# Optimization experiments

Measured on AMD Instinct MI355X. Metric: run time of the kernel, lower is better.

## Reference

```python
import jax, jax.numpy as jnp
import numpy as np

V, T, E, H, L = 32000, 1024, 1024, 16, 6
D = E // H
FF = 4 * E
B = 2


def _ln(x, s, b, eps=1e-5):
    m = x.mean(-1, keepdims=True)
    v = x.var(-1, keepdims=True)
    return (x - m) * jax.lax.rsqrt(v + eps) * s + b


def setup_inputs() -> dict:
    key = jax.random.key(0)
    ks = jax.random.split(key, 16)
    std = 0.02
    inp = {
        "idx": jax.random.randint(ks[0], (B, T), 0, V),
        "tok_w": jax.random.normal(ks[1], (V, E)) * std,
        "pos_emb": jax.random.normal(ks[2], (1, T, E)) * std,
        # stacked per-layer params [L, ...]
        "ln1_s": jnp.ones((L, E)), "ln1_b": jnp.zeros((L, E)),
        "wq": jax.random.normal(ks[3], (L, E, E)) * std,
        "wk": jax.random.normal(ks[4], (L, E, E)) * std,
        "wv": jax.random.normal(ks[5], (L, E, E)) * std,
        "wo": jax.random.normal(ks[6], (L, E, E)) * std,
        "bo": jnp.zeros((L, E)),
        "ln2_s": jnp.ones((L, E)), "ln2_b": jnp.zeros((L, E)),
        "w1": jax.random.normal(ks[7], (L, E, FF)) * std,
        "b1": jnp.zeros((L, FF)),
        "w2": jax.random.normal(ks[8], (L, FF, E)) * std,
        "b2": jnp.zeros((L, E)),
        "lnf_s": jnp.ones((E,)), "lnf_b": jnp.zeros((E,)),
        "head_w": jax.random.normal(ks[9], (E, V)) * std,
        "head_b": jnp.zeros((V,)),
    }
    return inp


def _gpt(idx, tok_w, pos_emb, ln1_s, ln1_b, wq, wk, wv, wo, bo,
         ln2_s, ln2_b, w1, b1, w2, b2, lnf_s, lnf_b, head_w, head_b):
    x = tok_w[idx] + pos_emb[0, :T]                      # [B,T,E]
    mask = jnp.tril(jnp.ones((T, T), dtype=bool))        # causal mask
    scale = 1.0 / np.sqrt(D)

    def step(x, p):
        l1s, l1b, q_w, k_w, v_w, o_w, o_b, l2s, l2b, f1, fb1, f2, fb2 = p
        h = _ln(x, l1s, l1b)
        q = (h @ q_w).reshape(B, T, H, D)
        k = (h @ k_w).reshape(B, T, H, D)
        v = (h @ v_w).reshape(B, T, H, D)
        att = jnp.einsum('bthd,bshd->bhts', q, k) * scale  # [B,H,T,T]
        att = jnp.where(mask, att, -jnp.inf)
        att = jax.nn.softmax(att, axis=-1)
        o = jnp.einsum('bhts,bshd->bthd', att, v).reshape(B, T, E)
        x = x + o @ o_w + o_b
        h2 = _ln(x, l2s, l2b)
        x = x + jax.nn.relu(h2 @ f1 + fb1) @ f2 + fb2
        return x, None

    params = (ln1_s, ln1_b, wq, wk, wv, wo, bo, ln2_s, ln2_b, w1, b1, w2, b2)
    x, _ = jax.lax.scan(step, x, params)
    x = _ln(x, lnf_s, lnf_b)
    return x @ head_w + head_b                           # logits [B,T,V]


def reference(idx, tok_w, pos_emb, ln1_s, ln1_b, wq, wk, wv, wo, bo,
              ln2_s, ln2_b, w1, b1, w2, b2, lnf_s, lnf_b, head_w, head_b):
    return _gpt(idx, tok_w, pos_emb, ln1_s, ln1_b, wq, wk, wv, wo, bo,
                ln2_s, ln2_b, w1, b1, w2, b2, lnf_s, lnf_b, head_w, head_b)
```

## Files before the change

### kernel.cpp

```cpp
#include <hip/hip_runtime.h>


#define T_SEQ 1024
#define E_DIM 1024
#define H_NUM 16
#define D_HEAD 64
#define L_NUM 6
#define FF_DIM 4096
#define B_NUM 2
#define M_ROWS 2048

using bf16x8 = __attribute__((ext_vector_type(8))) __bf16;
using f32x4  = __attribute__((ext_vector_type(4))) float;

__device__ __forceinline__ unsigned short f2bf(float f) {
  unsigned int u = __float_as_uint(f);
  u += 0x7fffu + ((u >> 16) & 1u);
  return (unsigned short)(u >> 16);
}

__device__ __forceinline__ void gload_lds16(const void* g, void* l) {
  __builtin_amdgcn_global_load_lds(
      (const __attribute__((address_space(1))) unsigned int*)g,
      (__attribute__((address_space(3))) unsigned int*)l, 16, 0, 0);
}

__global__ __launch_bounds__(256) void embed_k(const int* __restrict__ idx,
                                               const float* __restrict__ tok_w,
                                               const float* __restrict__ pos,
                                               float* __restrict__ x) {
  const int i = blockIdx.x;
  const int t = i & (T_SEQ - 1);
  const int tok = idx[i];
  const float4 a = ((const float4*)(tok_w + (size_t)tok * E_DIM))[threadIdx.x];
  const float4 p = ((const float4*)(pos + (size_t)t * E_DIM))[threadIdx.x];
  float4 o;
  o.x = a.x + p.x; o.y = a.y + p.y; o.z = a.z + p.z; o.w = a.w + p.w;
  ((float4*)(x + (size_t)i * E_DIM))[threadIdx.x] = o;
}

__global__ __launch_bounds__(256) void ln_k(const float* __restrict__ x,
                                            const float* __restrict__ s,
                                            const float* __restrict__ b,
                                            unsigned short* __restrict__ out) {
  const int row = blockIdx.x, tid = threadIdx.x;
  const float4 v = ((const float4*)(x + (size_t)row * E_DIM))[tid];
  float sum = v.x + v.y + v.z + v.w;
  float sq  = v.x * v.x + v.y * v.y + v.z * v.z + v.w * v.w;
  #pragma unroll
  for (int off = 32; off; off >>= 1) {
    sum += __shfl_down(sum, off);
    sq  += __shfl_down(sq, off);
  }
  __shared__ float sm[10];
  const int wave = tid >> 6, lane = tid & 63;
  if (lane == 0) { sm[wave] = sum; sm[4 + wave] = sq; }
  __syncthreads();
  if (tid == 0) {
    const float ts = sm[0] + sm[1] + sm[2] + sm[3];
    const float tq = sm[4] + sm[5] + sm[6] + sm[7];
    const float mean = ts * (1.0f / E_DIM);
    const float var = tq * (1.0f / E_DIM) - mean * mean;
    sm[8] = mean;
    sm[9] = 1.0f / sqrtf(var + 1e-5f);
  }
  __syncthreads();
  const float mean = sm[8], inv = sm[9];
  const float4 sv = ((const float4*)s)[tid];
  const float4 bv = ((const float4*)b)[tid];
  ushort4 o;
  o.x = f2bf((v.x - mean) * inv * sv.x + bv.x);
  o.y = f2bf((v.y - mean) * inv * sv.y + bv.y);
  o.z = f2bf((v.z - mean) * inv * sv.z + bv.z);
  o.w = f2bf((v.w - mean) * inv * sv.w + bv.w);
  *(ushort4*)(out + (size_t)row * E_DIM + (tid << 2)) = o;
}

__global__ __launch_bounds__(256) void transpose_k(const float* __restrict__ W,
                                                   unsigned short* __restrict__ WT,
                                                   int K, int ldw) {
  __shared__ float tile[32][33];
  const int n0 = blockIdx.x << 5, k0 = blockIdx.y << 5;
  const int tx = threadIdx.x & 31, ty = threadIdx.x >> 5;
  #pragma unroll
  for (int i = ty; i < 32; i += 8)
    tile[i][tx] = W[(size_t)(k0 + i) * ldw + n0 + tx];
  __syncthreads();
  #pragma unroll
  for (int i = ty; i < 32; i += 8)
    WT[(size_t)(n0 + i) * K + k0 + tx] = f2bf(tile[tx][i]);
}

template<int BM, bool RELU, bool BIAS, bool RES, bool OBF16>
__global__ __launch_bounds__(256) void gemm_k(const unsigned short* __restrict__ A,
                                              const unsigned short* __restrict__ WT,
                                              const float* __restrict__ bias,
                                              const float* __restrict__ res,
                                              void* __restrict__ Cout,
                                              int ldc, int K) {
  constexpr int BN = 128;
  constexpr int BK = 64;
  constexpr int MF = BM / 32;
  constexpr int AJ = (BM * BK * 2 / 1024) / 4;
  constexpr int BJ = (BN * BK * 2 / 1024) / 4;
  __shared__ __align__(16) unsigned short As[2][BM][BK];
  __shared__ __align__(16) unsigned short Bs[2][BN][BK];
  const int tid = threadIdx.x;
  const int row0 = blockIdx.x * BM, col0 = blockIdx.y * BN;
  const int wave = tid >> 6, lane = tid & 63;
  const int wm = (wave >> 1) * (BM / 2), wn = (wave & 1) * 64;
  const int lr = lane & 15, lg = lane >> 4;
  const int ric = lane >> 3;
  const int sslot = lane & 7;

  auto stage = [&](int buf, int k0) {
    #pragma unroll
    for (int j = 0; j < AJ; ++j) {
      const int c = wave + 4 * j;
      const int row = c * 8 + ric;
      const int sp = sslot ^ (row & 7);
      gload_lds16(A + (size_t)(row0 + row) * K + k0 + sp * 8,
                  (char*)&As[buf][0][0] + c * 1024);
    }
    #pragma unroll
    for (int j = 0; j < BJ; ++j) {
      const int c = wave + 4 * j;
      const int row = c * 8 + ric;
      const int sp = sslot ^ (row & 7);
      gload_lds16(WT + (size_t)(col0 + row) * K + k0 + sp * 8,
                  (char*)&Bs[buf][0][0] + c * 1024);
    }
  };

  f32x4 acc[MF][4] = {};
  const int nt = K / BK;
  stage(0, 0);
  __syncthreads();
  for (int t = 0; t < nt; ++t) {
    const int cur = t & 1;
    if (t + 1 < nt) stage(cur ^ 1, (t + 1) * BK);
    #pragma unroll
    for (int ks = 0; ks < 2; ++ks) {
      bf16x8 af[MF], bfr[4];
      #pragma unroll
      for (int m = 0; m < MF; ++m) {
        const int r = wm + m * 16 + lr;
        const int s = (ks * 4 + lg) ^ (r & 7);
        af[m] = *(const bf16x8*)((const char*)&As[cur][0][0] + r * 128 + s * 16);
      }
      #pragma unroll
      for (int n = 0; n < 4; ++n) {
        const int r = wn + n * 16 + lr;
        const int s = (ks * 4 + lg) ^ (r & 7);
        bfr[n] = *(const bf16x8*)((const char*)&Bs[cur][0][0] + r * 128 + s * 16);
      }
      #pragma unroll
      for (int m = 0; m < MF; ++m)
        #pragma unroll
        for (int n = 0; n < 4; ++n)
          acc[m][n] = __builtin_amdgcn_mfma_f32_16x16x32_bf16(af[m], bfr[n], acc[m][n], 0, 0, 0);
    }
    __syncthreads();
  }
  float* Cf = (float*)Cout;
  unsigned short* Cb = (unsigned short*)Cout;
  #pragma unroll
  for (int m = 0; m < MF; ++m) {
    #pragma unroll
    for (int n = 0; n < 4; ++n) {
      const int col = col0 + wn + (n << 4) + lr;
      const float bv = BIAS ? bias[col] : 0.0f;
      #pragma unroll
      for (int r = 0; r < 4; ++r) {
        const int row = row0 + wm + (m << 4) + (lg << 2) + r;
        float val = acc[m][n][r] + bv;
        if (RELU) val = fmaxf(val, 0.0f);
        if (RES)  val += res[(size_t)row * ldc + col];
        if (OBF16) Cb[(size_t)row * ldc + col] = f2bf(val);
        else       Cf[(size_t)row * ldc + col] = val;
      }
    }
  }
}

#define QBLK 64
#define KBLK 64
__global__ __launch_bounds__(256) void fattn_k(const unsigned short* __restrict__ qkv,
                                               unsigned short* __restrict__ ob) {
  const int qt = blockIdx.x, h = blockIdx.y, b = blockIdx.z;
  const int tid = threadIdx.x;
  const int wave = tid >> 6, lane = tid & 63;
  const int lr = lane & 15, lg = lane >> 4;
  const int q0 = qt * QBLK;

  __shared__ __align__(16) unsigned short Qs[QBLK][72];
  __shared__ __align__(16) unsigned short Ks[KBLK][72];
  __shared__ __align__(16) unsigned short Vt[D_HEAD][72];
  __shared__ __align__(16) unsigned short Ps[QBLK][72];

  const size_t base = (size_t)b * T_SEQ * 3072 + (size_t)h * 64;
  const int srow = tid >> 3, scol = (tid & 7) << 3;

  #pragma unroll
  for (int it = 0; it < 2; ++it) {
    const int row = srow + it * 32;
    *(uint4*)&Qs[row][scol] =
        *(const uint4*)(qkv + base + (size_t)(q0 + row) * 3072 + scol);
  }
  __syncthreads();
  bf16x8 qf[2];
  #pragma unroll
  for (int ks = 0; ks < 2; ++ks)
    qf[ks] = *(const bf16x8*)&Qs[wave * 16 + lr][ks * 32 + lg * 8];

  f32x4 acc_o[4] = {};
  float mrow[4], lrow[4];
  #pragma unroll
  for (int r = 0; r < 4; ++r) { mrow[r] = -3.0e38f; lrow[r] = 0.f; }

  const int ntile = qt + 1;
  for (int kt = 0; kt < ntile; ++kt) {
    const int s0 = kt * KBLK;
    __syncthreads();
    #pragma unroll
    for (int it = 0; it < 2; ++it) {
      const int row = srow + it * 32;
      *(uint4*)&Ks[row][scol] =
          *(const uint4*)(qkv + base + 1024 + (size_t)(s0 + row) * 3072 + scol);
      uint4 v4 = *(const uint4*)(qkv + base + 2048 + (size_t)(s0 + row) * 3072 + scol);
      const unsigned short* vs = (const unsigned short*)&v4;
      #pragma unroll
      for (int j = 0; j < 8; ++j) Vt[scol + j][row] = vs[j];
    }
    __syncthreads();

    f32x4 sacc[4] = {};
    #pragma unroll
    for (int ks = 0; ks < 2; ++ks) {
      #pragma unroll
      for (int nf = 0; nf < 4; ++nf) {
        bf16x8 kf = *(const bf16x8*)&Ks[nf * 16 + lr][ks * 32 + lg * 8];
        sacc[nf] = __builtin_amdgcn_mfma_f32_16x16x32_bf16(qf[ks], kf, sacc[nf], 0, 0, 0);
      }
    }
    float sv[4][4];
    #pragma unroll
    for (int nf = 0; nf < 4; ++nf)
      #pragma unroll
      for (int r = 0; r < 4; ++r) sv[nf][r] = sacc[nf][r] * 0.125f;
    if (kt == ntile - 1) {
      #pragma unroll
      for (int nf = 0; nf < 4; ++nf) {
        const int s = s0 + nf * 16 + lr;
        #pragma unroll
        for (int r = 0; r < 4; ++r) {
          const int q = q0 + wave * 16 + lg * 4 + r;
          if (s > q) sv[nf][r] = -3.0e38f;
        }
      }
    }
    float p[4][4];
    #pragma unroll
    for (int r = 0; r < 4; ++r) {
      float mx = fmaxf(fmaxf(sv[0][r], sv[1][r]), fmaxf(sv[2][r], sv[3][r]));
      #pragma unroll
      for (int off = 1; off < 16; off <<= 1) mx = fmaxf(mx, __shfl_xor(mx, off));
      const float mnew = fmaxf(mrow[r], mx);
      const float alpha = __expf(mrow[r] - mnew);
      mrow[r] = mnew;
      float sum = 0.f;
      #pragma unroll
      for (int nf = 0; nf < 4; ++nf) {
        p[nf][r] = __expf(sv[nf][r] - mnew);
        sum += p[nf][r];
      }
      #pragma unroll
      for (int off = 1; off < 16; off <<= 1) sum += __shfl_xor(sum, off);
      lrow[r] = lrow[r] * alpha + sum;
      #pragma unroll
      for (int df = 0; df < 4; ++df) acc_o[df][r] *= alpha;
    }
    #pragma unroll
    for (int nf = 0; nf < 4; ++nf)
      #pragma unroll
      for (int r = 0; r < 4; ++r)
        Ps[wave * 16 + lg * 4 + r][nf * 16 + lr] = f2bf(p[nf][r]);
    __syncthreads();
    #pragma unroll
    for (int ks = 0; ks < 2; ++ks) {
      bf16x8 pa = *(const bf16x8*)&Ps[wave * 16 + lr][ks * 32 + lg * 8];
      #pragma unroll
      for (int df = 0; df < 4; ++df) {
        bf16x8 vf = *(const bf16x8*)&Vt[df * 16 + lr][ks * 32 + lg * 8];
        acc_o[df] = __builtin_amdgcn_mfma_f32_16x16x32_bf16(pa, vf, acc_o[df], 0, 0, 0);
      }
    }
  }
  #pragma unroll
  for (int r = 0; r < 4; ++r) {
    const float inv = 1.0f / lrow[r];
    const int row = q0 + wave * 16 + lg * 4 + r;
    #pragma unroll
    for (int df = 0; df < 4; ++df)
      ob[((size_t)b * T_SEQ + row) * E_DIM + h * 64 + df * 16 + lr] =
          f2bf(acc_o[df][r] * inv);
  }
}

extern "C" void kernel_launch(void* const* d_in, const int* in_sizes, int n_in,
                              void* d_out, int out_size, void* d_ws, size_t ws_size,
                              hipStream_t stream) {
  (void)in_sizes; (void)n_in; (void)out_size; (void)ws_size;
  const int*   idx    = (const int*)d_in[0];
  const float* tok_w  = (const float*)d_in[1];
  const float* pos    = (const float*)d_in[2];
  const float* ln1_s  = (const float*)d_in[3];
  const float* ln1_b  = (const float*)d_in[4];
  const float* wq     = (const float*)d_in[5];
  const float* wk     = (const float*)d_in[6];
  const float* wv     = (const float*)d_in[7];
  const float* wo     = (const float*)d_in[8];
  const float* bo     = (const float*)d_in[9];
  const float* ln2_s  = (const float*)d_in[10];
  const float* ln2_b  = (const float*)d_in[11];
  const float* w1     = (const float*)d_in[12];
  const float* b1     = (const float*)d_in[13];
  const float* w2     = (const float*)d_in[14];
  const float* b2     = (const float*)d_in[15];
  const float* lnf_s  = (const float*)d_in[16];
  const float* lnf_b  = (const float*)d_in[17];
  const float* head_w = (const float*)d_in[18];
  const float* head_b = (const float*)d_in[19];
  float* out = (float*)d_out;

  char* p = (char*)d_ws;
  float* x            = (float*)p;          p += (size_t)M_ROWS * E_DIM * 4;
  unsigned short* qkvb= (unsigned short*)p; p += (size_t)M_ROWS * 3072 * 4;
  unsigned short* h   = (unsigned short*)p; p += (size_t)M_ROWS * E_DIM * 2;
  unsigned short* obuf= (unsigned short*)p; p += (size_t)M_ROWS * E_DIM * 2;
  unsigned short* ff  = (unsigned short*)p; p += (size_t)M_ROWS * FF_DIM * 2;
  unsigned short* wt  = (unsigned short*)p; p += (size_t)32000 * E_DIM * 2;

  embed_k<<<M_ROWS, 256, 0, stream>>>(idx, tok_w, pos, x);

  for (int l = 0; l < L_NUM; ++l) {
    const size_t lEE = (size_t)l * E_DIM * E_DIM;
    const size_t lEF = (size_t)l * E_DIM * FF_DIM;
    ln_k<<<M_ROWS, 256, 0, stream>>>(x, ln1_s + l * E_DIM, ln1_b + l * E_DIM, h);
    transpose_k<<<dim3(32, 32), 256, 0, stream>>>(wq + lEE, wt,               E_DIM, E_DIM);
    transpose_k<<<dim3(32, 32), 256, 0, stream>>>(wk + lEE, wt + 1048576,     E_DIM, E_DIM);
    transpose_k<<<dim3(32, 32), 256, 0, stream>>>(wv + lEE, wt + 2097152,     E_DIM, E_DIM);
    gemm_k<128,false,false,false,true><<<dim3(16, 24), 256, 0, stream>>>(
        h, wt, nullptr, nullptr, qkvb, 3072, E_DIM);
    fattn_k<<<dim3(T_SEQ / QBLK, H_NUM, B_NUM), 256, 0, stream>>>(qkvb, obuf);
    transpose_k<<<dim3(32, 32), 256, 0, stream>>>(wo + lEE, wt, E_DIM, E_DIM);
    gemm_k<64,false,true,true,false><<<dim3(32, 8), 256, 0, stream>>>(
        obuf, wt, bo + l * E_DIM, x, x, E_DIM, E_DIM);
    ln_k<<<M_ROWS, 256, 0, stream>>>(x, ln2_s + l * E_DIM, ln2_b + l * E_DIM, h);
    transpose_k<<<dim3(128, 32), 256, 0, stream>>>(w1 + lEF, wt, E_DIM, FF_DIM);
    gemm_k<128,true,true,false,true><<<dim3(16, 32), 256, 0, stream>>>(
        h, wt, b1 + l * FF_DIM, nullptr, ff, FF_DIM, E_DIM);
    transpose_k<<<dim3(32, 128), 256, 0, stream>>>(w2 + lEF, wt, FF_DIM, E_DIM);
    gemm_k<64,false,true,true,false><<<dim3(32, 8), 256, 0, stream>>>(
        ff, wt, b2 + l * E_DIM, x, x, E_DIM, FF_DIM);
  }

  ln_k<<<M_ROWS, 256, 0, stream>>>(x, lnf_s, lnf_b, h);
  transpose_k<<<dim3(1000, 32), 256, 0, stream>>>(head_w, wt, E_DIM, 32000);
  gemm_k<128,false,true,false,false><<<dim3(16, 250), 256, 0, stream>>>(
      h, wt, head_b, nullptr, out, 32000, E_DIM);
}
```

Before: 1.525 ms.

## Batch weight transposes up front and add 256x256 8-wave GEMM for LM head

All per-layer weight transposes are now done by batched launches (grid z over layers) before the layer loop, writing into dedicated per-layer transposed buffers instead of one reused scratch buffer. This cuts the number of small launches interleaved with compute. The LM head GEMM moves to a new 512-thread kernel with 256x256 tiles, quarter-split LDS double buffering, XCD-aware block remapping and MFMA priority hints, aimed at better operand reuse on the largest GEMM. The cost is a larger workspace and a more complex barrier and waitcnt schedule that must hold across the split stages.

```diff
diff --git a/kernel.cpp b/kernel.cpp
--- a/kernel.cpp
+++ b/kernel.cpp
@@ -76,15 +76,19 @@
   *(ushort4*)(out + (size_t)row * E_DIM + (tid << 2)) = o;
 }
 
-__global__ __launch_bounds__(256) void transpose_k(const float* __restrict__ W,
+__global__ __launch_bounds__(256) void transpose_b(const float* __restrict__ W,
                                                    unsigned short* __restrict__ WT,
-                                                   int K, int ldw) {
+                                                   int K, int N,
+                                                   size_t Wstride, size_t WTstride) {
   __shared__ float tile[32][33];
+  const int z = blockIdx.z;
+  W  += (size_t)z * Wstride;
+  WT += (size_t)z * WTstride;
   const int n0 = blockIdx.x << 5, k0 = blockIdx.y << 5;
   const int tx = threadIdx.x & 31, ty = threadIdx.x >> 5;
   #pragma unroll
   for (int i = ty; i < 32; i += 8)
-    tile[i][tx] = W[(size_t)(k0 + i) * ldw + n0 + tx];
+    tile[i][tx] = W[(size_t)(k0 + i) * N + n0 + tx];
   __syncthreads();
   #pragma unroll
   for (int i = ty; i < 32; i += 8)
@@ -110,8 +114,7 @@
   const int wave = tid >> 6, lane = tid & 63;
   const int wm = (wave >> 1) * (BM / 2), wn = (wave & 1) * 64;
   const int lr = lane & 15, lg = lane >> 4;
-  const int ric = lane >> 3;
-  const int sslot = lane & 7;
+  const int ric = lane >> 3, sslot = lane & 7;
 
   auto stage = [&](int buf, int k0) {
     #pragma unroll
@@ -181,6 +184,135 @@
       }
     }
   }
+}
+
+#define LOAD_AF(HALF)                                                         \
+  _Pragma("unroll")                                                           \
+  for (int mf = 0; mf < 4; ++mf) {                                            \
+    const int rr = wm * 64 + mf * 16 + lr;                                    \
+    _Pragma("unroll")                                                         \
+    for (int ks = 0; ks < 2; ++ks)                                            \
+      af[mf][ks] = *(const bf16x8*)&As[buf][HALF][rr]                         \
+          [(((ks << 2) + lgp) ^ (rr & 7)) << 3];                              \
+  }
+#define LOAD_BF(HALF)                                                         \
+  _Pragma("unroll")                                                           \
+  for (int nf = 0; nf < 2; ++nf) {                                            \
+    const int rr = wn * 32 + nf * 16 + lr;                                    \
+    _Pragma("unroll")                                                         \
+    for (int ks = 0; ks < 2; ++ks)                                            \
+      bfq[nf][ks] = *(const bf16x8*)&Bs[buf][HALF][rr]                        \
+          [(((ks << 2) + lgp) ^ (rr & 7)) << 3];                              \
+  }
+#define MFMA_Q(MH, NH)                                                        \
+  __builtin_amdgcn_s_setprio(1);                                              \
+  _Pragma("unroll")                                                           \
+  for (int mf = 0; mf < 4; ++mf)                                              \
+    _Pragma("unroll")                                                         \
+    for (int nf = 0; nf < 2; ++nf) {                                          \
+      acc[MH][NH][mf][nf] = __builtin_amdgcn_mfma_f32_16x16x32_bf16(          \
+          af[mf][0], bfq[nf][0], acc[MH][NH][mf][nf], 0, 0, 0);               \
+      acc[MH][NH][mf][nf] = __builtin_amdgcn_mfma_f32_16x16x32_bf16(          \
+          af[mf][1], bfq[nf][1], acc[MH][NH][mf][nf], 0, 0, 0);               \
+    }                                                                         \
+  __builtin_amdgcn_s_setprio(0);
+
+__global__ __launch_bounds__(512) void gemm8_k(
+    const unsigned short* __restrict__ A, const unsigned short* __restrict__ WT,
+    const float* __restrict__ bias, float* __restrict__ C,
+    int ldc, int K, int mgrid) {
+  constexpr int BK = 64;
+  __shared__ __align__(16) unsigned short As[2][2][128][64];
+  __shared__ __align__(16) unsigned short Bs[2][2][128][64];
+  const int tid = threadIdx.x;
+  const int wave = tid >> 6, lane = tid & 63;
+  const int wm = wave >> 2, wn = wave & 3;
+  const int lr = lane & 15, lgp = lane >> 4;
+  const int nwg = gridDim.x;
+  const int q = nwg >> 3, r = nwg & 7;
+  const int xcd = blockIdx.x & 7;
+  const int lgid = (xcd < r ? xcd * (q + 1) : r * (q + 1) + (xcd - r) * q)
+                   + (blockIdx.x >> 3);
+  const int row0 = (lgid % mgrid) * 256, col0 = (lgid / mgrid) * 256;
+  const int srow = lane >> 3, sslot = lane & 7;
+
+  auto stA = [&](int buf, int half, int k0) {
+    #pragma unroll
+    for (int j = 0; j < 2; ++j) {
+      const int row = j * 64 + wave * 8 + srow;
+      const int sp = sslot ^ (row & 7);
+      gload_lds16(A + (size_t)(row0 + half * 128 + row) * K + k0 + sp * 8,
+                  (char*)&As[buf][half][0][0] + j * 8192 + wave * 1024);
+    }
+  };
+  auto stB = [&](int buf, int half, int k0) {
+    #pragma unroll
+    for (int j = 0; j < 2; ++j) {
+      const int row = j * 64 + wave * 8 + srow;
+      const int sp = sslot ^ (row & 7);
+      gload_lds16(WT + (size_t)(col0 + half * 128 + row) * K + k0 + sp * 8,
+                  (char*)&Bs[buf][half][0][0] + j * 8192 + wave * 1024);
+    }
+  };
+
+  f32x4 acc[2][2][4][2] = {};
+  bf16x8 af[4][2], bfq[2][2];
+  const int nt = K / BK;
+
+  stA(0, 0, 0); stB(0, 1, 0); stB(0, 0, 0); stA(0, 1, 0);
+  if (nt > 1) {
+    stA(1, 0, BK); stB(1, 1, BK);
+    asm volatile("s_waitcnt vmcnt(4)" ::: "memory");
+  } else {
+    asm volatile("s_waitcnt vmcnt(0)" ::: "memory");
+  }
+  __builtin_amdgcn_s_barrier();
+
+  for (int t = 0; t < nt; ++t) {
+    const int buf = t & 1, nbuf = buf ^ 1;
+    const int k0 = t * BK;
+    LOAD_AF(0)
+    LOAD_BF(0)
+    if (t + 1 < nt) { stB(nbuf, 0, k0 + BK); stA(nbuf, 1, k0 + BK); }
+    __builtin_amdgcn_s_barrier();
+    MFMA_Q(0, 0)
+    __builtin_amdgcn_s_barrier();
+    LOAD_BF(1)
+    __builtin_amdgcn_s_barrier();
+    MFMA_Q(0, 1)
+    __builtin_amdgcn_s_barrier();
+    LOAD_AF(1)
+    if (t + 2 < nt) stA(buf, 0, k0 + 2 * BK);
+    __builtin_amdgcn_s_barrier();
+    MFMA_Q(1, 1)
+    __builtin_amdgcn_s_barrier();
+    LOAD_BF(0)
+    if (t + 2 < nt) stB(buf, 1, k0 + 2 * BK);
+    __builtin_amdgcn_s_barrier();
+    MFMA_Q(1, 0)
+    if (t + 1 < nt) {
+      if (t + 2 < nt) asm volatile("s_waitcnt vmcnt(4)" ::: "memory");
+      else            asm volatile("s_waitcnt vmcnt(0)" ::: "memory");
+    }
+    __builtin_amdgcn_s_barrier();
+  }
+
+  #pragma unroll
+  for (int mh = 0; mh < 2; ++mh)
+    #pragma unroll
+    for (int nh = 0; nh < 2; ++nh)
+      #pragma unroll
+      for (int mf = 0; mf < 4; ++mf)
+        #pragma unroll
+        for (int nf = 0; nf < 2; ++nf) {
+          const int col = col0 + nh * 128 + wn * 32 + nf * 16 + lr;
+          const float bv = bias[col];
+          #pragma unroll
+          for (int rr = 0; rr < 4; ++rr) {
+            const int row = row0 + mh * 128 + wm * 64 + mf * 16 + lgp * 4 + rr;
+            C[(size_t)row * ldc + col] = acc[mh][nh][mf][nf][rr] + bv;
+          }
+        }
 }
 
 #define QBLK 64
@@ -335,38 +467,47 @@
 
   char* p = (char*)d_ws;
   float* x            = (float*)p;          p += (size_t)M_ROWS * E_DIM * 4;
-  unsigned short* qkvb= (unsigned short*)p; p += (size_t)M_ROWS * 3072 * 4;
+  unsigned short* qkvb= (unsigned short*)p; p += (size_t)M_ROWS * 3072 * 2;
   unsigned short* h   = (unsigned short*)p; p += (size_t)M_ROWS * E_DIM * 2;
   unsigned short* obuf= (unsigned short*)p; p += (size_t)M_ROWS * E_DIM * 2;
   unsigned short* ff  = (unsigned short*)p; p += (size_t)M_ROWS * FF_DIM * 2;
-  unsigned short* wt  = (unsigned short*)p; p += (size_t)32000 * E_DIM * 2;
+  unsigned short* wtqkv=(unsigned short*)p; p += (size_t)L_NUM * 3072 * E_DIM * 2;
+  unsigned short* wto = (unsigned short*)p; p += (size_t)L_NUM * E_DIM * E_DIM * 2;
+  unsigned short* wt1 = (unsigned short*)p; p += (size_t)L_NUM * FF_DIM * E_DIM * 2;
+  unsigned short* wt2 = (unsigned short*)p; p += (size_t)L_NUM * E_DIM * FF_DIM * 2;
+  unsigned short* wth = (unsigned short*)p; p += (size_t)32000 * E_DIM * 2;
+
+  transpose_b<<<dim3(32, 32, L_NUM), 256, 0, stream>>>(
+      wq, wtqkv,           E_DIM, E_DIM, (size_t)E_DIM * E_DIM, (size_t)3072 * E_DIM);
+  transpose_b<<<dim3(32, 32, L_NUM), 256, 0, stream>>>(
+      wk, wtqkv + 1048576, E_DIM, E_DIM, (size_t)E_DIM * E_DIM, (size_t)3072 * E_DIM);
+  transpose_b<<<dim3(32, 32, L_NUM), 256, 0, stream>>>(
+      wv, wtqkv + 2097152, E_DIM, E_DIM, (size_t)E_DIM * E_DIM, (size_t)3072 * E_DIM);
+  transpose_b<<<dim3(32, 32, L_NUM), 256, 0, stream>>>(
+      wo, wto, E_DIM, E_DIM, (size_t)E_DIM * E_DIM, (size_t)E_DIM * E_DIM);
+  transpose_b<<<dim3(128, 32, L_NUM), 256, 0, stream>>>(
+      w1, wt1, E_DIM, FF_DIM, (size_t)E_DIM * FF_DIM, (size_t)FF_DIM * E_DIM);
+  transpose_b<<<dim3(32, 128, L_NUM), 256, 0, stream>>>(
+      w2, wt2, FF_DIM, E_DIM, (size_t)E_DIM * FF_DIM, (size_t)E_DIM * FF_DIM);
+  transpose_b<<<dim3(1000, 32, 1), 256, 0, stream>>>(
+      head_w, wth, E_DIM, 32000, 0, 0);
 
   embed_k<<<M_ROWS, 256, 0, stream>>>(idx, tok_w, pos, x);
 
   for (int l = 0; l < L_NUM; ++l) {
-    const size_t lEE = (size_t)l * E_DIM * E_DIM;
-    const size_t lEF = (size_t)l * E_DIM * FF_DIM;
     ln_k<<<M_ROWS, 256, 0, stream>>>(x, ln1_s + l * E_DIM, ln1_b + l * E_DIM, h);
-    transpose_k<<<dim3(32, 32), 256, 0, stream>>>(wq + lEE, wt,               E_DIM, E_DIM);
-    transpose_k<<<dim3(32, 32), 256, 0, stream>>>(wk + lEE, wt + 1048576,     E_DIM, E_DIM);
-    transpose_k<<<dim3(32, 32), 256, 0, stream>>>(wv + lEE, wt + 2097152,     E_DIM, E_DIM);
     gemm_k<128,false,false,false,true><<<dim3(16, 24), 256, 0, stream>>>(
-        h, wt, nullptr, nullptr, qkvb, 3072, E_DIM);
+        h, wtqkv + (size_t)l * 3072 * E_DIM, nullptr, nullptr, qkvb, 3072, E_DIM);
     fattn_k<<<dim3(T_SEQ / QBLK, H_NUM, B_NUM), 256, 0, stream>>>(qkvb, obuf);
-    transpose_k<<<dim3(32, 32), 256, 0, stream>>>(wo + lEE, wt, E_DIM, E_DIM);
     gemm_k<64,false,true,true,false><<<dim3(32, 8), 256, 0, stream>>>(
-        obuf, wt, bo + l * E_DIM, x, x, E_DIM, E_DIM);
+        obuf, wto + (size_t)l * E_DIM * E_DIM, bo + l * E_DIM, x, x, E_DIM, E_DIM);
     ln_k<<<M_ROWS, 256, 0, stream>>>(x, ln2_s + l * E_DIM, ln2_b + l * E_DIM, h);
-    transpose_k<<<dim3(128, 32), 256, 0, stream>>>(w1 + lEF, wt, E_DIM, FF_DIM);
     gemm_k<128,true,true,false,true><<<dim3(16, 32), 256, 0, stream>>>(
-        h, wt, b1 + l * FF_DIM, nullptr, ff, FF_DIM, E_DIM);
-    transpose_k<<<dim3(32, 128), 256, 0, stream>>>(w2 + lEF, wt, FF_DIM, E_DIM);
+        h, wt1 + (size_t)l * FF_DIM * E_DIM, b1 + l * FF_DIM, nullptr, ff, FF_DIM, E_DIM);
     gemm_k<64,false,true,true,false><<<dim3(32, 8), 256, 0, stream>>>(
-        ff, wt, b2 + l * E_DIM, x, x, E_DIM, FF_DIM);
+        ff, wt2 + (size_t)l * E_DIM * FF_DIM, b2 + l * E_DIM, x, x, E_DIM, FF_DIM);
   }
 
   ln_k<<<M_ROWS, 256, 0, stream>>>(x, lnf_s, lnf_b, h);
-  transpose_k<<<dim3(1000, 32), 256, 0, stream>>>(head_w, wt, E_DIM, 32000);
-  gemm_k<128,false,true,false,false><<<dim3(16, 250), 256, 0, stream>>>(
-      h, wt, head_b, nullptr, out, 32000, E_DIM);
-}
+  gemm8_k<<<1000, 512, 0, stream>>>(h, wth, head_b, out, 32000, E_DIM, 8);
+}
```

Result: slower. 1.594 ms (+4.5%).
